# Kernel tuning notes

Hardware: AMD Instinct MI355X
Metric: run time of the kernel (lower is better)

Reference implementation:

```python
import jax, jax.numpy as jnp
import numpy as np

B, H, W, Z = 4, 256, 256, 64
ITERATIONS = 8
EPSILON = 1e-06
CENTER = 6.0  # 7-point Laplacian diagonal


def _stencil(x):
    # x: [B, H, W, Z]; zero (Dirichlet) boundaries via padded shifts
    west = jnp.pad(x[:, :, :-1, :], ((0, 0), (0, 0), (1, 0), (0, 0)))
    east = jnp.pad(x[:, :, 1:, :], ((0, 0), (0, 0), (0, 1), (0, 0)))
    north = jnp.pad(x[:, :-1, :, :], ((0, 0), (1, 0), (0, 0), (0, 0)))
    south = jnp.pad(x[:, 1:, :, :], ((0, 0), (0, 1), (0, 0), (0, 0)))
    bottom = jnp.pad(x[:, :, :, :-1], ((0, 0), (0, 0), (0, 0), (1, 0)))
    top = jnp.pad(x[:, :, :, 1:], ((0, 0), (0, 0), (0, 0), (0, 1)))
    return CENTER * x - west - east - south - north - bottom - top


def _dot(a, b):
    # per-sample dot product, keepdims for scalar broadcast
    return jnp.sum(a * b, axis=(1, 2, 3), keepdims=True)


def setup_inputs() -> dict:
    key = jax.random.key(0)
    k1, k2, k3 = jax.random.split(key, 3)
    shape = (B, H, W, Z)
    return {
        "x": jax.random.normal(k1, shape, dtype=jnp.float32),
        "b": jax.random.normal(k2, shape, dtype=jnp.float32),
        "reference_sol": jax.random.normal(k3, shape, dtype=jnp.float32),
    }


def reference(x, b, reference_sol):
    r = b - _stencil(x)
    p = r
    rho = _dot(r, r)

    def body(carry, _):
        x, r, p, rho = carry
        w = _stencil(p)
        eta = _dot(p, w)
        alpha = rho / (eta + EPSILON)
        x = x + alpha * p
        r = r - alpha * w
        rho_next = _dot(r, r)
        beta = rho_next / (rho + EPSILON)
        p = r + beta * p
        return (x, r, p, rho_next), None

    (x, r, p, rho), _ = jax.lax.scan(body, (x, r, p, rho), None, length=ITERATIONS)

    diff = x - reference_sol
    loss = jnp.mean(diff * diff)
    max_error = jnp.max(jnp.abs(diff))
    residual_norm_sq = jnp.mean(rho)
    return (loss, x, max_error, residual_norm_sq)
```

## Files before the change

### kernel.cpp

```cpp
#include <hip/hip_runtime.h>

#define B_ 4
#define H_ 256
#define W_ 256
#define Z_ 64
#define NB_ (H_*W_*Z_)
#define N_  (B_*NB_)
#define ITER_ 8
#define EPS_ 1e-6f
#define SLOTS_ 64

#define RHO_OFF   0
#define ETA_OFF   ((ITER_+1)*B_*SLOTS_)
#define LOSS_OFF  (ETA_OFF + ITER_*B_*SLOTS_)
#define MAXE_OFF  (LOSS_OFF + SLOTS_)
#define SCAL_FLOATS (MAXE_OFF + SLOTS_)

struct F8 { float4 a, b; };

__device__ __forceinline__ float wsum(float v){
  v += __shfl_xor(v,32); v += __shfl_xor(v,16); v += __shfl_xor(v,8);
  v += __shfl_xor(v,4);  v += __shfl_xor(v,2);  v += __shfl_xor(v,1);
  return v;
}
__device__ __forceinline__ float wmaxr(float v){
  v = fmaxf(v,__shfl_xor(v,32)); v = fmaxf(v,__shfl_xor(v,16));
  v = fmaxf(v,__shfl_xor(v,8));  v = fmaxf(v,__shfl_xor(v,4));
  v = fmaxf(v,__shfl_xor(v,2));  v = fmaxf(v,__shfl_xor(v,1));
  return v;
}
__device__ __forceinline__ float read_sum(const float* s){
  return wsum(s[threadIdx.x & 63]);
}
__device__ __forceinline__ void block_atomic_sum(float v, float* dst, float* lds){
  v = wsum(v);
  int wid = threadIdx.x >> 6, lane = threadIdx.x & 63;
  if (lane == 0) lds[wid] = v;
  __syncthreads();
  if (threadIdx.x == 0) atomicAdd(dst, lds[0]+lds[1]+lds[2]+lds[3]);
}

__device__ __forceinline__ float4 ld4(const float* p){ return *(const float4*)p; }

__device__ __forceinline__ void sten_core(const F8& c, const F8& wm, const F8& wp,
                                          const F8& hm, const F8& hp,
                                          float zl, float zr, F8& st)
{
  st.a.x = 6.f*c.a.x - wm.a.x - wp.a.x - hm.a.x - hp.a.x - zl     - c.a.y;
  st.a.y = 6.f*c.a.y - wm.a.y - wp.a.y - hm.a.y - hp.a.y - c.a.x  - c.a.z;
  st.a.z = 6.f*c.a.z - wm.a.z - wp.a.z - hm.a.z - hp.a.z - c.a.y  - c.a.w;
  st.a.w = 6.f*c.a.w - wm.a.w - wp.a.w - hm.a.w - hp.a.w - c.a.z  - c.b.x;
  st.b.x = 6.f*c.b.x - wm.b.x - wp.b.x - hm.b.x - hp.b.x - c.a.w  - c.b.y;
  st.b.y = 6.f*c.b.y - wm.b.y - wp.b.y - hm.b.y - hp.b.y - c.b.x  - c.b.z;
  st.b.z = 6.f*c.b.z - wm.b.z - wp.b.z - hm.b.z - hp.b.z - c.b.y  - c.b.w;
  st.b.w = 6.f*c.b.w - wm.b.w - wp.b.w - hm.b.w - hp.b.w - c.b.z  - zr;
}

__device__ __forceinline__ void stencil1(const float* __restrict__ a, int base,
                                         int w, int h, int zc, F8& c, F8& st)
{
  c.a = ld4(a+base); c.b = ld4(a+base+4);
  F8 zero; zero.a = make_float4(0,0,0,0); zero.b = zero.a;
  F8 wm = zero, wp = zero, hm = zero, hp = zero;
  if (w > 0)    { wm.a = ld4(a+base-Z_);    wm.b = ld4(a+base-Z_+4); }
  if (w < W_-1) { wp.a = ld4(a+base+Z_);    wp.b = ld4(a+base+Z_+4); }
  if (h > 0)    { hm.a = ld4(a+base-W_*Z_); hm.b = ld4(a+base-W_*Z_+4); }
  if (h < H_-1) { hp.a = ld4(a+base+W_*Z_); hp.b = ld4(a+base+W_*Z_+4); }
  float zl = (zc > 0) ? a[base-1] : 0.f;
  float zr = (zc < 7) ? a[base+8] : 0.f;
  sten_core(c, wm, wp, hm, hp, zl, zr, st);
}

__device__ __forceinline__ F8 comb8(const float* r, const float* p, float beta, int idx){
  F8 o;
  float4 ra = ld4(r+idx), rb = ld4(r+idx+4);
  float4 pa = ld4(p+idx), pb = ld4(p+idx+4);
  o.a.x = ra.x + beta*pa.x; o.a.y = ra.y + beta*pa.y;
  o.a.z = ra.z + beta*pa.z; o.a.w = ra.w + beta*pa.w;
  o.b.x = rb.x + beta*pb.x; o.b.y = rb.y + beta*pb.y;
  o.b.z = rb.z + beta*pb.z; o.b.w = rb.w + beta*pb.w;
  return o;
}
__device__ __forceinline__ void stencil2(const float* __restrict__ r,
                                         const float* __restrict__ p, float beta,
                                         int base, int w, int h, int zc,
                                         F8& c, F8& st)
{
  c = comb8(r,p,beta,base);
  F8 zero; zero.a = make_float4(0,0,0,0); zero.b = zero.a;
  F8 wm = zero, wp = zero, hm = zero, hp = zero;
  if (w > 0)    wm = comb8(r,p,beta,base-Z_);
  if (w < W_-1) wp = comb8(r,p,beta,base+Z_);
  if (h > 0)    hm = comb8(r,p,beta,base-W_*Z_);
  if (h < H_-1) hp = comb8(r,p,beta,base+W_*Z_);
  float zl = (zc > 0) ? r[base-1] + beta*p[base-1] : 0.f;
  float zr = (zc < 7) ? r[base+8] + beta*p[base+8] : 0.f;
  sten_core(c, wm, wp, hm, hp, zl, zr, st);
}

#define IDX_SETUP \
  const int zc = threadIdx.x & 7; \
  const int wl = threadIdx.x >> 3; \
  const int w  = blockIdx.x*32 + wl; \
  const int h  = blockIdx.y; \
  const int bb = blockIdx.z; \
  const int base = ((bb*H_ + h)*W_ + w)*Z_ + zc*8; \
  const int flat = (blockIdx.z*gridDim.y + blockIdx.y)*gridDim.x + blockIdx.x; \
  const int slot = flat & (SLOTS_-1);

__global__ __launch_bounds__(256) void k_init(const float* __restrict__ x,
                                              const float* __restrict__ b,
                                              float* __restrict__ r,
                                              float* scal)
{
  __shared__ float lds[4];
  IDX_SETUP
  F8 c, st;
  stencil1(x, base, w, h, zc, c, st);
  float4 b0 = ld4(b+base), b1 = ld4(b+base+4);
  F8 rv;
  rv.a = make_float4(b0.x-st.a.x, b0.y-st.a.y, b0.z-st.a.z, b0.w-st.a.w);
  rv.b = make_float4(b1.x-st.b.x, b1.y-st.b.y, b1.z-st.b.z, b1.w-st.b.w);
  *(float4*)(r+base)   = rv.a;
  *(float4*)(r+base+4) = rv.b;
  float rho = rv.a.x*rv.a.x + rv.a.y*rv.a.y + rv.a.z*rv.a.z + rv.a.w*rv.a.w
            + rv.b.x*rv.b.x + rv.b.y*rv.b.y + rv.b.z*rv.b.z + rv.b.w*rv.b.w;
  block_atomic_sum(rho, scal + RHO_OFF + (0*B_+bb)*SLOTS_ + slot, lds);
}

__global__ __launch_bounds__(256) void k_a0(const float* __restrict__ r,
                                            float* __restrict__ pnew,
                                            float* scal)
{
  __shared__ float lds[4];
  IDX_SETUP
  F8 c, st;
  stencil1(r, base, w, h, zc, c, st);
  *(float4*)(pnew+base)   = c.a;
  *(float4*)(pnew+base+4) = c.b;
  float eta = c.a.x*st.a.x + c.a.y*st.a.y + c.a.z*st.a.z + c.a.w*st.a.w
            + c.b.x*st.b.x + c.b.y*st.b.y + c.b.z*st.b.z + c.b.w*st.b.w;
  block_atomic_sum(eta, scal + ETA_OFF + (0*B_+bb)*SLOTS_ + slot, lds);
}

__global__ __launch_bounds__(256) void k_a(const float* __restrict__ r,
                                           const float* __restrict__ pold,
                                           float* __restrict__ pnew,
                                           float* scal, int it)
{
  __shared__ float lds[4];
  IDX_SETUP
  float num = read_sum(scal + RHO_OFF + (it*B_+bb)*SLOTS_);
  float den = read_sum(scal + RHO_OFF + ((it-1)*B_+bb)*SLOTS_);
  float beta = num / (den + EPS_);
  F8 c, st;
  stencil2(r, pold, beta, base, w, h, zc, c, st);
  *(float4*)(pnew+base)   = c.a;
  *(float4*)(pnew+base+4) = c.b;
  float eta = c.a.x*st.a.x + c.a.y*st.a.y + c.a.z*st.a.z + c.a.w*st.a.w
            + c.b.x*st.b.x + c.b.y*st.b.y + c.b.z*st.b.z + c.b.w*st.b.w;
  block_atomic_sum(eta, scal + ETA_OFF + (it*B_+bb)*SLOTS_ + slot, lds);
}

__global__ __launch_bounds__(256) void k_b(float* __restrict__ x,
                                           float* __restrict__ r,
                                           const float* __restrict__ p,
                                           float* scal, int it)
{
  __shared__ float lds[4];
  IDX_SETUP
  float num = read_sum(scal + RHO_OFF + (it*B_+bb)*SLOTS_);
  float den = read_sum(scal + ETA_OFF + (it*B_+bb)*SLOTS_);
  float alpha = num / (den + EPS_);
  F8 c, st;
  stencil1(p, base, w, h, zc, c, st);
  float4 x0 = ld4(x+base), x1 = ld4(x+base+4);
  x0.x += alpha*c.a.x; x0.y += alpha*c.a.y; x0.z += alpha*c.a.z; x0.w += alpha*c.a.w;
  x1.x += alpha*c.b.x; x1.y += alpha*c.b.y; x1.z += alpha*c.b.z; x1.w += alpha*c.b.w;
  *(float4*)(x+base)   = x0;
  *(float4*)(x+base+4) = x1;
  float4 r0 = ld4(r+base), r1 = ld4(r+base+4);
  r0.x -= alpha*st.a.x; r0.y -= alpha*st.a.y; r0.z -= alpha*st.a.z; r0.w -= alpha*st.a.w;
  r1.x -= alpha*st.b.x; r1.y -= alpha*st.b.y; r1.z -= alpha*st.b.z; r1.w -= alpha*st.b.w;
  *(float4*)(r+base)   = r0;
  *(float4*)(r+base+4) = r1;
  float rho = r0.x*r0.x + r0.y*r0.y + r0.z*r0.z + r0.w*r0.w
            + r1.x*r1.x + r1.y*r1.y + r1.z*r1.z + r1.w*r1.w;
  block_atomic_sum(rho, scal + RHO_OFF + ((it+1)*B_+bb)*SLOTS_ + slot, lds);
}

__global__ __launch_bounds__(256) void k_b_fin(const float* __restrict__ x,
                                               const float* __restrict__ r,
                                               const float* __restrict__ p,
                                               const float* __restrict__ ref,
                                               float* __restrict__ out,
                                               float* scal, int it)
{
  __shared__ float xs[2048];
  __shared__ float lds[12];
  IDX_SETUP
  float num = read_sum(scal + RHO_OFF + (it*B_+bb)*SLOTS_);
  float den = read_sum(scal + ETA_OFF + (it*B_+bb)*SLOTS_);
  float alpha = num / (den + EPS_);
  F8 c, st;
  stencil1(p, base, w, h, zc, c, st);
  float4 x0 = ld4(x+base), x1 = ld4(x+base+4);
  x0.x += alpha*c.a.x; x0.y += alpha*c.a.y; x0.z += alpha*c.a.z; x0.w += alpha*c.a.w;
  x1.x += alpha*c.b.x; x1.y += alpha*c.b.y; x1.z += alpha*c.b.z; x1.w += alpha*c.b.w;
  float4 r0 = ld4(r+base), r1 = ld4(r+base+4);
  r0.x -= alpha*st.a.x; r0.y -= alpha*st.a.y; r0.z -= alpha*st.a.z; r0.w -= alpha*st.a.w;
  r1.x -= alpha*st.b.x; r1.y -= alpha*st.b.y; r1.z -= alpha*st.b.z; r1.w -= alpha*st.b.w;
  float rho = r0.x*r0.x + r0.y*r0.y + r0.z*r0.z + r0.w*r0.w
            + r1.x*r1.x + r1.y*r1.y + r1.z*r1.z + r1.w*r1.w;

  const int t = threadIdx.x;
  xs[t*8+0] = x0.x; xs[t*8+1] = x0.y; xs[t*8+2] = x0.z; xs[t*8+3] = x0.w;
  xs[t*8+4] = x1.x; xs[t*8+5] = x1.y; xs[t*8+6] = x1.z; xs[t*8+7] = x1.w;

  float4 f0 = ld4(ref+base), f1 = ld4(ref+base+4);
  float d0 = x0.x-f0.x, d1 = x0.y-f0.y, d2 = x0.z-f0.z, d3 = x0.w-f0.w;
  float d4 = x1.x-f1.x, d5 = x1.y-f1.y, d6 = x1.z-f1.z, d7 = x1.w-f1.w;
  float loss = d0*d0+d1*d1+d2*d2+d3*d3+d4*d4+d5*d5+d6*d6+d7*d7;
  float me = fmaxf(fmaxf(fmaxf(fabsf(d0),fabsf(d1)),fmaxf(fabsf(d2),fabsf(d3))),
                   fmaxf(fmaxf(fabsf(d4),fabsf(d5)),fmaxf(fabsf(d6),fabsf(d7))));

  float rs = wsum(rho), ls = wsum(loss), ms = wmaxr(me);
  int wid = t >> 6, lane = t & 63;
  if (lane == 0) { lds[wid] = rs; lds[4+wid] = ls; lds[8+wid] = ms; }
  __syncthreads();
  if (t == 0) {
    atomicAdd(scal + RHO_OFF + ((it+1)*B_+bb)*SLOTS_ + slot, lds[0]+lds[1]+lds[2]+lds[3]);
    atomicAdd(scal + LOSS_OFF + slot, lds[4]+lds[5]+lds[6]+lds[7]);
    float bm = fmaxf(fmaxf(lds[8],lds[9]), fmaxf(lds[10],lds[11]));
    atomicMax((unsigned int*)(scal + MAXE_OFF) + slot, __float_as_uint(bm));
  }

  const int S = flat * 2048;
  #pragma unroll
  for (int c2 = 0; c2 < 2; ++c2) {
    int q = t + 256*c2;
    if (q < 511) {
      float4 v = make_float4(xs[3+4*q], xs[4+4*q], xs[5+4*q], xs[6+4*q]);
      *(float4*)(out + S + 4 + 4*q) = v;
    } else if (q == 511) {
      out[S+1] = xs[0]; out[S+2] = xs[1]; out[S+3] = xs[2];
      out[S+2048] = xs[2047];
    }
  }
}

__global__ __launch_bounds__(64) void k_scal(const float* scal, float* out)
{
  int lane = threadIdx.x;
  float loss = wsum(scal[LOSS_OFF + lane]);
  float me   = wmaxr(__uint_as_float(((const unsigned int*)scal)[MAXE_OFF + lane]));
  float rho_sum = 0.f;
  for (int bb = 0; bb < B_; ++bb)
    rho_sum += wsum(scal[RHO_OFF + (ITER_*B_+bb)*SLOTS_ + lane]);
  if (lane == 0) {
    out[0]      = loss / (float)N_;
    out[1+N_]   = me;
    out[2+N_]   = rho_sum / (float)B_;
  }
}

extern "C" void kernel_launch(void* const* d_in, const int* in_sizes, int n_in,
                              void* d_out, int out_size, void* d_ws, size_t ws_size,
                              hipStream_t stream) {
  float* x         = (float*)d_in[0];
  const float* b   = (const float*)d_in[1];
  const float* ref = (const float*)d_in[2];
  float* out       = (float*)d_out;

  float* r  = (float*)d_ws;
  float* p0 = r + N_;
  float* p1;
  float* scal;
  size_t need3 = ((size_t)3*N_ + SCAL_FLOATS) * sizeof(float);
  if (ws_size >= need3) {
    p1   = p0 + N_;
    scal = p1 + N_;
  } else {
    p1   = (float*)d_out;
    scal = p0 + N_;
  }

  (void)hipMemsetAsync(scal, 0, SCAL_FLOATS*sizeof(float), stream);

  dim3 grid(W_/32, H_, B_), blk(256);
  k_init<<<grid, blk, 0, stream>>>(x, b, r, scal);

  float* pa = p1;
  float* pb = p0;
  for (int it = 0; it < ITER_; ++it) {
    if (it == 0)
      k_a0<<<grid, blk, 0, stream>>>(r, pa, scal);
    else
      k_a<<<grid, blk, 0, stream>>>(r, pb, pa, scal, it);
    if (it < ITER_-1)
      k_b<<<grid, blk, 0, stream>>>(x, r, pa, scal, it);
    else
      k_b_fin<<<grid, blk, 0, stream>>>(x, r, pa, ref, out, scal, it);
    float* t = pa; pa = pb; pb = t;
  }

  k_scal<<<1, 64, 0, stream>>>(scal, out);
}
```

Measured before the change: 1.097 ms.

## Shuffle z-neighbours, skip p copy at iteration zero, fold final scalar kernel

The z-direction neighbours now come from wavefront lane shuffles instead of extra global loads. Neighbour subtraction is restructured to accumulate incrementally, which reduces live registers. The first iteration uses r directly as p, avoiding a full-array copy, and rotates buffers so r is kept in a separate workspace slot. Inputs read once and the final output stores are nontemporal, the LDS staging is padded to avoid bank conflicts, and the last k_b_fin block computes the scalar outputs through an atomic ticket, which removes the separate k_scal launch. The risks are that the ticket ordering needs correct memory visibility and that the buffer aliasing becomes more complex.

```diff
diff --git a/kernel.cpp b/kernel.cpp
--- a/kernel.cpp
+++ b/kernel.cpp
@@ -9,14 +9,27 @@
 #define ITER_ 8
 #define EPS_ 1e-6f
 #define SLOTS_ 64
+#define NTILE_ 8192
 
 #define RHO_OFF   0
 #define ETA_OFF   ((ITER_+1)*B_*SLOTS_)
 #define LOSS_OFF  (ETA_OFF + ITER_*B_*SLOTS_)
 #define MAXE_OFF  (LOSS_OFF + SLOTS_)
-#define SCAL_FLOATS (MAXE_OFF + SLOTS_)
+#define TICK_OFF  (MAXE_OFF + SLOTS_)
+#define SCAL_FLOATS (TICK_OFF + 32)
 
 struct F8 { float4 a, b; };
+
+typedef float vf4 __attribute__((ext_vector_type(4)));
+
+__device__ __forceinline__ float4 ldnt4(const float* p){
+  vf4 v = __builtin_nontemporal_load((const vf4*)p);
+  return make_float4(v.x, v.y, v.z, v.w);
+}
+__device__ __forceinline__ void stnt4(float* p, float4 v){
+  vf4 t; t.x = v.x; t.y = v.y; t.z = v.z; t.w = v.w;
+  __builtin_nontemporal_store(t, (vf4*)p);
+}
 
 __device__ __forceinline__ float wsum(float v){
   v += __shfl_xor(v,32); v += __shfl_xor(v,16); v += __shfl_xor(v,8);
@@ -42,33 +55,36 @@
 
 __device__ __forceinline__ float4 ld4(const float* p){ return *(const float4*)p; }
 
-__device__ __forceinline__ void sten_core(const F8& c, const F8& wm, const F8& wp,
-                                          const F8& hm, const F8& hp,
-                                          float zl, float zr, F8& st)
-{
-  st.a.x = 6.f*c.a.x - wm.a.x - wp.a.x - hm.a.x - hp.a.x - zl     - c.a.y;
-  st.a.y = 6.f*c.a.y - wm.a.y - wp.a.y - hm.a.y - hp.a.y - c.a.x  - c.a.z;
-  st.a.z = 6.f*c.a.z - wm.a.z - wp.a.z - hm.a.z - hp.a.z - c.a.y  - c.a.w;
-  st.a.w = 6.f*c.a.w - wm.a.w - wp.a.w - hm.a.w - hp.a.w - c.a.z  - c.b.x;
-  st.b.x = 6.f*c.b.x - wm.b.x - wp.b.x - hm.b.x - hp.b.x - c.a.w  - c.b.y;
-  st.b.y = 6.f*c.b.y - wm.b.y - wp.b.y - hm.b.y - hp.b.y - c.b.x  - c.b.z;
-  st.b.z = 6.f*c.b.z - wm.b.z - wp.b.z - hm.b.z - hp.b.z - c.b.y  - c.b.w;
-  st.b.w = 6.f*c.b.w - wm.b.w - wp.b.w - hm.b.w - hp.b.w - c.b.z  - zr;
+__device__ __forceinline__ void sub8(F8& s, const F8& n){
+  s.a.x-=n.a.x; s.a.y-=n.a.y; s.a.z-=n.a.z; s.a.w-=n.a.w;
+  s.b.x-=n.b.x; s.b.y-=n.b.y; s.b.z-=n.b.z; s.b.w-=n.b.w;
+}
+
+__device__ __forceinline__ void zcore(const F8& c, int zc, F8& st){
+  float zl = __shfl_up(c.b.w, 1);
+  float zr = __shfl_down(c.a.x, 1);
+  zl = (zc > 0) ? zl : 0.f;
+  zr = (zc < 7) ? zr : 0.f;
+  st.a.x = 6.f*c.a.x - zl    - c.a.y;
+  st.a.y = 6.f*c.a.y - c.a.x - c.a.z;
+  st.a.z = 6.f*c.a.z - c.a.y - c.a.w;
+  st.a.w = 6.f*c.a.w - c.a.z - c.b.x;
+  st.b.x = 6.f*c.b.x - c.a.w - c.b.y;
+  st.b.y = 6.f*c.b.y - c.b.x - c.b.z;
+  st.b.z = 6.f*c.b.z - c.b.y - c.b.w;
+  st.b.w = 6.f*c.b.w - c.b.z - zr;
 }
 
 __device__ __forceinline__ void stencil1(const float* __restrict__ a, int base,
                                          int w, int h, int zc, F8& c, F8& st)
 {
   c.a = ld4(a+base); c.b = ld4(a+base+4);
-  F8 zero; zero.a = make_float4(0,0,0,0); zero.b = zero.a;
-  F8 wm = zero, wp = zero, hm = zero, hp = zero;
-  if (w > 0)    { wm.a = ld4(a+base-Z_);    wm.b = ld4(a+base-Z_+4); }
-  if (w < W_-1) { wp.a = ld4(a+base+Z_);    wp.b = ld4(a+base+Z_+4); }
-  if (h > 0)    { hm.a = ld4(a+base-W_*Z_); hm.b = ld4(a+base-W_*Z_+4); }
-  if (h < H_-1) { hp.a = ld4(a+base+W_*Z_); hp.b = ld4(a+base+W_*Z_+4); }
-  float zl = (zc > 0) ? a[base-1] : 0.f;
-  float zr = (zc < 7) ? a[base+8] : 0.f;
-  sten_core(c, wm, wp, hm, hp, zl, zr, st);
+  zcore(c, zc, st);
+  F8 t;
+  if (w > 0)    { t.a = ld4(a+base-Z_);    t.b = ld4(a+base-Z_+4);    sub8(st,t); }
+  if (w < W_-1) { t.a = ld4(a+base+Z_);    t.b = ld4(a+base+Z_+4);    sub8(st,t); }
+  if (h > 0)    { t.a = ld4(a+base-W_*Z_); t.b = ld4(a+base-W_*Z_+4); sub8(st,t); }
+  if (h < H_-1) { t.a = ld4(a+base+W_*Z_); t.b = ld4(a+base+W_*Z_+4); sub8(st,t); }
 }
 
 __device__ __forceinline__ F8 comb8(const float* r, const float* p, float beta, int idx){
@@ -87,15 +103,16 @@
                                          F8& c, F8& st)
 {
   c = comb8(r,p,beta,base);
-  F8 zero; zero.a = make_float4(0,0,0,0); zero.b = zero.a;
-  F8 wm = zero, wp = zero, hm = zero, hp = zero;
-  if (w > 0)    wm = comb8(r,p,beta,base-Z_);
-  if (w < W_-1) wp = comb8(r,p,beta,base+Z_);
-  if (h > 0)    hm = comb8(r,p,beta,base-W_*Z_);
-  if (h < H_-1) hp = comb8(r,p,beta,base+W_*Z_);
-  float zl = (zc > 0) ? r[base-1] + beta*p[base-1] : 0.f;
-  float zr = (zc < 7) ? r[base+8] + beta*p[base+8] : 0.f;
-  sten_core(c, wm, wp, hm, hp, zl, zr, st);
+  zcore(c, zc, st);
+  if (w > 0)    sub8(st, comb8(r,p,beta,base-Z_));
+  if (w < W_-1) sub8(st, comb8(r,p,beta,base+Z_));
+  if (h > 0)    sub8(st, comb8(r,p,beta,base-W_*Z_));
+  if (h < H_-1) sub8(st, comb8(r,p,beta,base+W_*Z_));
+}
+
+__device__ __forceinline__ float dot8(const F8& a, const F8& b){
+  return a.a.x*b.a.x + a.a.y*b.a.y + a.a.z*b.a.z + a.a.w*b.a.w
+       + a.b.x*b.b.x + a.b.y*b.b.y + a.b.z*b.b.z + a.b.w*b.b.w;
 }
 
 #define IDX_SETUP \
@@ -108,6 +125,8 @@
   const int flat = (blockIdx.z*gridDim.y + blockIdx.y)*gridDim.x + blockIdx.x; \
   const int slot = flat & (SLOTS_-1);
 
+#define XI(k) ((((k) >> 3)*9) + ((k) & 7))
+
 __global__ __launch_bounds__(256) void k_init(const float* __restrict__ x,
                                               const float* __restrict__ b,
                                               float* __restrict__ r,
@@ -117,15 +136,14 @@
   IDX_SETUP
   F8 c, st;
   stencil1(x, base, w, h, zc, c, st);
-  float4 b0 = ld4(b+base), b1 = ld4(b+base+4);
+  float4 b0 = ldnt4(b+base);
+  float4 b1 = ldnt4(b+base+4);
   F8 rv;
   rv.a = make_float4(b0.x-st.a.x, b0.y-st.a.y, b0.z-st.a.z, b0.w-st.a.w);
   rv.b = make_float4(b1.x-st.b.x, b1.y-st.b.y, b1.z-st.b.z, b1.w-st.b.w);
   *(float4*)(r+base)   = rv.a;
   *(float4*)(r+base+4) = rv.b;
-  float rho = rv.a.x*rv.a.x + rv.a.y*rv.a.y + rv.a.z*rv.a.z + rv.a.w*rv.a.w
-            + rv.b.x*rv.b.x + rv.b.y*rv.b.y + rv.b.z*rv.b.z + rv.b.w*rv.b.w;
-  block_atomic_sum(rho, scal + RHO_OFF + (0*B_+bb)*SLOTS_ + slot, lds);
+  block_atomic_sum(dot8(rv,rv), scal + RHO_OFF + (0*B_+bb)*SLOTS_ + slot, lds);
 }
 
 __global__ __launch_bounds__(256) void k_a0(const float* __restrict__ r,
@@ -136,11 +154,8 @@
   IDX_SETUP
   F8 c, st;
   stencil1(r, base, w, h, zc, c, st);
-  *(float4*)(pnew+base)   = c.a;
-  *(float4*)(pnew+base+4) = c.b;
-  float eta = c.a.x*st.a.x + c.a.y*st.a.y + c.a.z*st.a.z + c.a.w*st.a.w
-            + c.b.x*st.b.x + c.b.y*st.b.y + c.b.z*st.b.z + c.b.w*st.b.w;
-  block_atomic_sum(eta, scal + ETA_OFF + (0*B_+bb)*SLOTS_ + slot, lds);
+  if (pnew) { *(float4*)(pnew+base) = c.a; *(float4*)(pnew+base+4) = c.b; }
+  block_atomic_sum(dot8(c,st), scal + ETA_OFF + (0*B_+bb)*SLOTS_ + slot, lds);
 }
 
 __global__ __launch_bounds__(256) void k_a(const float* __restrict__ r,
@@ -157,14 +172,13 @@
   stencil2(r, pold, beta, base, w, h, zc, c, st);
   *(float4*)(pnew+base)   = c.a;
   *(float4*)(pnew+base+4) = c.b;
-  float eta = c.a.x*st.a.x + c.a.y*st.a.y + c.a.z*st.a.z + c.a.w*st.a.w
-            + c.b.x*st.b.x + c.b.y*st.b.y + c.b.z*st.b.z + c.b.w*st.b.w;
-  block_atomic_sum(eta, scal + ETA_OFF + (it*B_+bb)*SLOTS_ + slot, lds);
+  block_atomic_sum(dot8(c,st), scal + ETA_OFF + (it*B_+bb)*SLOTS_ + slot, lds);
 }
 
 __global__ __launch_bounds__(256) void k_b(float* __restrict__ x,
-                                           float* __restrict__ r,
-                                           const float* __restrict__ p,
+                                           const float* r_in,
+                                           float* r_out,
+                                           const float* p,
                                            float* scal, int it)
 {
   __shared__ float lds[4];
@@ -179,11 +193,11 @@
   x1.x += alpha*c.b.x; x1.y += alpha*c.b.y; x1.z += alpha*c.b.z; x1.w += alpha*c.b.w;
   *(float4*)(x+base)   = x0;
   *(float4*)(x+base+4) = x1;
-  float4 r0 = ld4(r+base), r1 = ld4(r+base+4);
+  float4 r0 = ld4(r_in+base), r1 = ld4(r_in+base+4);
   r0.x -= alpha*st.a.x; r0.y -= alpha*st.a.y; r0.z -= alpha*st.a.z; r0.w -= alpha*st.a.w;
   r1.x -= alpha*st.b.x; r1.y -= alpha*st.b.y; r1.z -= alpha*st.b.z; r1.w -= alpha*st.b.w;
-  *(float4*)(r+base)   = r0;
-  *(float4*)(r+base+4) = r1;
+  *(float4*)(r_out+base)   = r0;
+  *(float4*)(r_out+base+4) = r1;
   float rho = r0.x*r0.x + r0.y*r0.y + r0.z*r0.z + r0.w*r0.w
             + r1.x*r1.x + r1.y*r1.y + r1.z*r1.z + r1.w*r1.w;
   block_atomic_sum(rho, scal + RHO_OFF + ((it+1)*B_+bb)*SLOTS_ + slot, lds);
@@ -196,9 +210,11 @@
                                                float* __restrict__ out,
                                                float* scal, int it)
 {
-  __shared__ float xs[2048];
+  __shared__ float xs[256*9];
   __shared__ float lds[12];
-  IDX_SETUP
+  __shared__ unsigned is_last;
+  IDX_SETUP
+  const int t = threadIdx.x;
   float num = read_sum(scal + RHO_OFF + (it*B_+bb)*SLOTS_);
   float den = read_sum(scal + ETA_OFF + (it*B_+bb)*SLOTS_);
   float alpha = num / (den + EPS_);
@@ -213,11 +229,11 @@
   float rho = r0.x*r0.x + r0.y*r0.y + r0.z*r0.z + r0.w*r0.w
             + r1.x*r1.x + r1.y*r1.y + r1.z*r1.z + r1.w*r1.w;
 
-  const int t = threadIdx.x;
-  xs[t*8+0] = x0.x; xs[t*8+1] = x0.y; xs[t*8+2] = x0.z; xs[t*8+3] = x0.w;
-  xs[t*8+4] = x1.x; xs[t*8+5] = x1.y; xs[t*8+6] = x1.z; xs[t*8+7] = x1.w;
-
-  float4 f0 = ld4(ref+base), f1 = ld4(ref+base+4);
+  xs[t*9+0] = x0.x; xs[t*9+1] = x0.y; xs[t*9+2] = x0.z; xs[t*9+3] = x0.w;
+  xs[t*9+4] = x1.x; xs[t*9+5] = x1.y; xs[t*9+6] = x1.z; xs[t*9+7] = x1.w;
+
+  float4 f0 = ldnt4(ref+base);
+  float4 f1 = ldnt4(ref+base+4);
   float d0 = x0.x-f0.x, d1 = x0.y-f0.y, d2 = x0.z-f0.z, d3 = x0.w-f0.w;
   float d4 = x1.x-f1.x, d5 = x1.y-f1.y, d6 = x1.z-f1.z, d7 = x1.w-f1.w;
   float loss = d0*d0+d1*d1+d2*d2+d3*d3+d4*d4+d5*d5+d6*d6+d7*d7;
@@ -233,6 +249,10 @@
     atomicAdd(scal + LOSS_OFF + slot, lds[4]+lds[5]+lds[6]+lds[7]);
     float bm = fmaxf(fmaxf(lds[8],lds[9]), fmaxf(lds[10],lds[11]));
     atomicMax((unsigned int*)(scal + MAXE_OFF) + slot, __float_as_uint(bm));
+    asm volatile("s_waitcnt vmcnt(0)" ::: "memory");
+    unsigned old = __hip_atomic_fetch_add((unsigned*)(scal + TICK_OFF), 1u,
+                                          __ATOMIC_RELAXED, __HIP_MEMORY_SCOPE_AGENT);
+    is_last = (old == NTILE_-1) ? 1u : 0u;
   }
 
   const int S = flat * 2048;
@@ -240,27 +260,31 @@
   for (int c2 = 0; c2 < 2; ++c2) {
     int q = t + 256*c2;
     if (q < 511) {
-      float4 v = make_float4(xs[3+4*q], xs[4+4*q], xs[5+4*q], xs[6+4*q]);
-      *(float4*)(out + S + 4 + 4*q) = v;
+      int k = 4*q + 3;
+      float4 v = make_float4(xs[XI(k)], xs[XI(k+1)], xs[XI(k+2)], xs[XI(k+3)]);
+      stnt4(out + S + 4 + 4*q, v);
     } else if (q == 511) {
-      out[S+1] = xs[0]; out[S+2] = xs[1]; out[S+3] = xs[2];
-      out[S+2048] = xs[2047];
+      out[S+1] = xs[XI(0)]; out[S+2] = xs[XI(1)]; out[S+3] = xs[XI(2)];
+      out[S+2048] = xs[XI(2047)];
     }
   }
-}
-
-__global__ __launch_bounds__(64) void k_scal(const float* scal, float* out)
-{
-  int lane = threadIdx.x;
-  float loss = wsum(scal[LOSS_OFF + lane]);
-  float me   = wmaxr(__uint_as_float(((const unsigned int*)scal)[MAXE_OFF + lane]));
-  float rho_sum = 0.f;
-  for (int bb = 0; bb < B_; ++bb)
-    rho_sum += wsum(scal[RHO_OFF + (ITER_*B_+bb)*SLOTS_ + lane]);
-  if (lane == 0) {
-    out[0]      = loss / (float)N_;
-    out[1+N_]   = me;
-    out[2+N_]   = rho_sum / (float)B_;
+
+  __syncthreads();
+  if (is_last && t < 64) {
+    float lossv = wsum(__hip_atomic_load(scal + LOSS_OFF + t,
+                                         __ATOMIC_RELAXED, __HIP_MEMORY_SCOPE_AGENT));
+    unsigned mu = __hip_atomic_load((unsigned*)scal + MAXE_OFF + t,
+                                    __ATOMIC_RELAXED, __HIP_MEMORY_SCOPE_AGENT);
+    float mev = wmaxr(__uint_as_float(mu));
+    float rho_sum = 0.f;
+    for (int b2 = 0; b2 < B_; ++b2)
+      rho_sum += wsum(__hip_atomic_load(scal + RHO_OFF + (ITER_*B_+b2)*SLOTS_ + t,
+                                        __ATOMIC_RELAXED, __HIP_MEMORY_SCOPE_AGENT));
+    if (t == 0) {
+      out[0]    = lossv / (float)N_;
+      out[1+N_] = mev;
+      out[2+N_] = rho_sum / (float)B_;
+    }
   }
 }
 
@@ -268,41 +292,51 @@
                               void* d_out, int out_size, void* d_ws, size_t ws_size,
                               hipStream_t stream) {
   float* x         = (float*)d_in[0];
-  const float* b   = (const float*)d_in[1];
+  const float* bv  = (const float*)d_in[1];
   const float* ref = (const float*)d_in[2];
   float* out       = (float*)d_out;
-
-  float* r  = (float*)d_ws;
-  float* p0 = r + N_;
-  float* p1;
-  float* scal;
-  size_t need3 = ((size_t)3*N_ + SCAL_FLOATS) * sizeof(float);
-  if (ws_size >= need3) {
-    p1   = p0 + N_;
-    scal = p1 + N_;
+  float* ws        = (float*)d_ws;
+
+  dim3 grid(W_/32, H_, B_), blk(256);
+  bool fast = ws_size >= ((size_t)3*N_ + SCAL_FLOATS) * sizeof(float);
+
+  if (fast) {
+    float* R0 = ws;
+    float* R1 = ws + N_;
+    float* P0 = ws + 2*(size_t)N_;
+    float* P1 = out;
+    float* scal = ws + 3*(size_t)N_;
+    (void)hipMemsetAsync(scal, 0, SCAL_FLOATS*sizeof(float), stream);
+
+    k_init<<<grid, blk, 0, stream>>>(x, bv, R0, scal);
+    k_a0  <<<grid, blk, 0, stream>>>(R0, nullptr, scal);
+    k_b   <<<grid, blk, 0, stream>>>(x, R0, R1, R0, scal, 0);
+    float* pa = P0; float* pb = R0;
+    for (int it = 1; it < ITER_; ++it) {
+      k_a<<<grid, blk, 0, stream>>>(R1, pb, pa, scal, it);
+      if (it < ITER_-1)
+        k_b<<<grid, blk, 0, stream>>>(x, R1, R1, pa, scal, it);
+      else
+        k_b_fin<<<grid, blk, 0, stream>>>(x, R1, pa, ref, out, scal, it);
+      pb = pa; pa = (pa == P0) ? P1 : P0;
+    }
   } else {
-    p1   = (float*)d_out;
-    scal = p0 + N_;
+    float* r    = ws;
+    float* p0w  = ws + N_;
+    float* scal = ws + 2*(size_t)N_;
+    (void)hipMemsetAsync(scal, 0, SCAL_FLOATS*sizeof(float), stream);
+
+    k_init<<<grid, blk, 0, stream>>>(x, bv, r, scal);
+    k_a0  <<<grid, blk, 0, stream>>>(r, out, scal);
+    k_b   <<<grid, blk, 0, stream>>>(x, r, r, out, scal, 0);
+    float* pa = p0w; float* pb = out;
+    for (int it = 1; it < ITER_; ++it) {
+      k_a<<<grid, blk, 0, stream>>>(r, pb, pa, scal, it);
+      if (it < ITER_-1)
+        k_b<<<grid, blk, 0, stream>>>(x, r, r, pa, scal, it);
+      else
+        k_b_fin<<<grid, blk, 0, stream>>>(x, r, pa, ref, out, scal, it);
+      pb = pa; pa = (pa == p0w) ? out : p0w;
+    }
   }
-
-  (void)hipMemsetAsync(scal, 0, SCAL_FLOATS*sizeof(float), stream);
-
-  dim3 grid(W_/32, H_, B_), blk(256);
-  k_init<<<grid, blk, 0, stream>>>(x, b, r, scal);
-
-  float* pa = p1;
-  float* pb = p0;
-  for (int it = 0; it < ITER_; ++it) {
-    if (it == 0)
-      k_a0<<<grid, blk, 0, stream>>>(r, pa, scal);
-    else
-      k_a<<<grid, blk, 0, stream>>>(r, pb, pa, scal, it);
-    if (it < ITER_-1)
-      k_b<<<grid, blk, 0, stream>>>(x, r, pa, scal, it);
-    else
-      k_b_fin<<<grid, blk, 0, stream>>>(x, r, pa, ref, out, scal, it);
-    float* t = pa; pa = pb; pb = t;
-  }
-
-  k_scal<<<1, 64, 0, stream>>>(scal, out);
-}
+}
```

New measurement: 1.118 ms. About the same (+1.9%).
